# Kernel tuning notes

Hardware: AMD Instinct MI355X
Metric: run time of the kernel (lower is better)

## Reference

```python
import jax, jax.numpy as jnp
import numpy as np

PRE = 4096      # NMS_PRE_MAXSIZE
POST = 512      # NMS_POST_MAXSIZE
THRESH = 0.7    # NMS_THRESH


def setup_inputs() -> dict:
    key = jax.random.key(0)
    k1, k2, k3, k4, k5 = jax.random.split(key, 5)
    B, N, C = 4, 32768, 3
    # realistic lidar-frame boxes: (x, y, z, dx, dy, dz, heading)
    xy = jax.random.uniform(k1, (B, N, 2)) * 140.0 - 70.0
    z = jax.random.uniform(k2, (B, N, 1)) * 3.0 - 2.0
    dims = jax.random.uniform(k3, (B, N, 3)) * 4.0 + 1.0
    heading = jax.random.uniform(k4, (B, N, 1)) * (2.0 * np.pi) - np.pi
    batch_box_preds = jnp.concatenate([xy, z, dims, heading], axis=-1)
    batch_cls_preds = jax.random.normal(k5, (B, N, C))
    return {"batch_cls_preds": batch_cls_preds, "batch_box_preds": batch_box_preds}


def _bev_iou(boxes):
    # boxes: (K, 7); axis-aligned BEV IoU over (x, y, dx, dy) -> (K, K)
    x, y, dx, dy = boxes[:, 0], boxes[:, 1], boxes[:, 3], boxes[:, 4]
    x1, x2 = x - dx * 0.5, x + dx * 0.5
    y1, y2 = y - dy * 0.5, y + dy * 0.5
    ix = jnp.clip(jnp.minimum(x2[:, None], x2[None, :]) - jnp.maximum(x1[:, None], x1[None, :]), 0.0)
    iy = jnp.clip(jnp.minimum(y2[:, None], y2[None, :]) - jnp.maximum(y1[:, None], y1[None, :]), 0.0)
    inter = ix * iy
    area = dx * dy
    union = area[:, None] + area[None, :] - inter
    return inter / jnp.maximum(union, 1e-6)


def _class_agnostic_nms(scores, boxes):
    # scores: (N,), boxes: (N, 7) -> selected idx (POST,), scores (POST,), valid (POST,)
    topk_scores, idx = jax.lax.top_k(scores, PRE)          # score-sorted candidates
    iou = _bev_iou(boxes[idx])                              # (PRE, PRE)
    ar = jnp.arange(PRE)
    def body(i, keep):  # greedy suppression in score order
        sup = keep[i] & (iou[i] > THRESH) & (ar > i)
        return keep & ~sup
    keep = jax.lax.fori_loop(0, PRE, body, jnp.ones((PRE,), bool))
    order = jnp.argsort(jnp.where(keep, ar, PRE))           # stable: kept first, score order
    sel = order[:POST]
    valid = keep[sel]
    return idx[sel], topk_scores[sel] * valid, valid


def reference(batch_cls_preds, batch_box_preds):
    # argmax scoring over classes (torch.max(cls_preds, dim=1))
    roi_scores_all = jnp.max(batch_cls_preds, axis=-1)      # (B, N)
    roi_labels_all = jnp.argmax(batch_cls_preds, axis=-1)   # (B, N)

    def per_item(scores, labels, boxes):
        sel, sel_scores, valid = _class_agnostic_nms(scores, boxes)
        rois = boxes[sel] * valid[:, None].astype(boxes.dtype)   # zero-padded buffer
        roi_labels = jnp.where(valid, labels[sel], 0) + 1        # +1 applied to whole buffer
        return rois, sel_scores, roi_labels

    rois, roi_scores, roi_labels = jax.vmap(per_item)(roi_scores_all, roi_labels_all, batch_box_preds)
    return rois, roi_scores, roi_labels
```

## Files before the change

### kernel.cpp

```cpp
#include <hip/hip_runtime.h>
#include <stdint.h>

typedef unsigned long long u64;

#define BB 4
#define NN 32768
#define CC 3
#define PRE 4096
#define RNK 768
#define POST 512
#define TH 0.7f
#define ROWS_A 768
#define RW (ROWS_A / 64)
#define CANDCAP 2048
#define RS_TILE 2048

__device__ __forceinline__ uint32_t f2u(float f) {
    uint32_t b = __float_as_uint(f);
    return (b & 0x80000000u) ? ~b : (b | 0x80000000u);
}
__device__ __forceinline__ float u2f(uint32_t u) {
    uint32_t b = (u & 0x80000000u) ? (u & 0x7FFFFFFFu) : ~u;
    return __uint_as_float(b);
}
__device__ __forceinline__ float score3(const float* p) {
    return fmaxf(fmaxf(p[0], p[1]), p[2]);
}

__global__ void k_zero(uint4* __restrict__ histreg, uint32_t* __restrict__ scal, int n16) {
    int gid = blockIdx.x * blockDim.x + threadIdx.x;
    if (gid < n16) histreg[gid] = make_uint4(0, 0, 0, 0);
    if (gid < 16) scal[gid] = 0;
}

__global__ void k_hist(const float* __restrict__ cls,
                       uint32_t* __restrict__ hist_f, uint32_t* __restrict__ hist_c) {
    __shared__ uint32_t lc[256];
    lc[threadIdx.x] = 0;
    __syncthreads();
    int gid = blockIdx.x * blockDim.x + threadIdx.x;
    int b = gid >> 15;
    uint32_t p16 = f2u(score3(cls + (size_t)gid * CC)) >> 16;
    atomicAdd(&hist_f[((uint32_t)b << 16) + p16], 1u);
    atomicAdd(&lc[p16 >> 8], 1u);
    __syncthreads();
    uint32_t v = lc[threadIdx.x];
    if (v) atomicAdd(&hist_c[((uint32_t)b << 8) + threadIdx.x], v);
}

__global__ void __launch_bounds__(256) k_collect(const float* __restrict__ cls,
                                                 const uint32_t* __restrict__ hist_c,
                                                 const uint32_t* __restrict__ hist_f,
                                                 uint32_t* __restrict__ cnt,
                                                 uint32_t* __restrict__ ccnt,
                                                 u64* __restrict__ selk, u64* __restrict__ cand) {
    int tid = threadIdx.x;
    int gid = blockIdx.x * 256 + tid;
    int b = gid >> 15;
    __shared__ uint32_t pref[256];
    __shared__ uint32_t s_selc, s_remc, s_pb;

    uint32_t v = hist_c[((uint32_t)b << 8) + 255 - tid];
    pref[tid] = v;
    __syncthreads();
    for (int off = 1; off < 256; off <<= 1) {
        uint32_t x = (tid >= off) ? pref[tid - off] : 0;
        __syncthreads();
        pref[tid] += x;
        __syncthreads();
    }
    {
        uint32_t after = pref[tid], before = after - v;
        if (before < RNK && RNK <= after) { s_selc = 255 - tid; s_remc = RNK - before; }
    }
    __syncthreads();
    uint32_t selc = s_selc, remc = s_remc;
    uint32_t v2 = hist_f[((uint32_t)b << 16) + (selc << 8) + 255 - tid];
    __syncthreads();
    pref[tid] = v2;
    __syncthreads();
    for (int off = 1; off < 256; off <<= 1) {
        uint32_t x = (tid >= off) ? pref[tid - off] : 0;
        __syncthreads();
        pref[tid] += x;
        __syncthreads();
    }
    {
        uint32_t after = pref[tid], before = after - v2;
        if (before < remc && remc <= after) s_pb = (selc << 8) | (uint32_t)(255 - tid);
    }
    __syncthreads();
    uint32_t pb = s_pb;

    u64 k = ((u64)f2u(score3(cls + (size_t)gid * CC)) << 32)
          | (uint32_t)(~(uint32_t)(gid & (NN - 1)));
    uint32_t p16 = (uint32_t)(k >> 48);
    bool def = p16 > pb;
    u64 mask = __ballot(def);
    int lane = tid & 63;
    int wave = tid >> 6;
    __shared__ uint32_t wtot[4], wbase[4], blockbase;
    uint32_t rank = lane ? (uint32_t)__popcll(mask & ((~0ull) >> (64 - lane))) : 0u;
    if (lane == 0) wtot[wave] = (uint32_t)__popcll(mask);
    __syncthreads();
    if (tid == 0) {
        uint32_t t = 0;
        for (int w = 0; w < 4; ++w) { wbase[w] = t; t += wtot[w]; }
        blockbase = atomicAdd(&cnt[b], t);
    }
    __syncthreads();
    if (def) {
        selk[(size_t)b * RNK + blockbase + wbase[wave] + rank] = k;
    } else if (p16 == pb) {
        uint32_t pos = atomicAdd(&ccnt[b], 1u);
        if (pos < CANDCAP) cand[(size_t)b * CANDCAP + pos] = k;
    }
}

__global__ void __launch_bounds__(256) k_rankscatter(const u64* __restrict__ selk,
                                                     const u64* __restrict__ cand,
                                                     const uint32_t* __restrict__ cnt,
                                                     const uint32_t* __restrict__ ccnt,
                                                     const float* __restrict__ box,
                                                     int* __restrict__ sidx,
                                                     float* __restrict__ ssc,
                                                     float* __restrict__ bf) {
    const int bpi = RS_TILE / 64;
    int b = blockIdx.x / bpi;
    int c = blockIdx.x % bpi;
    uint32_t base = cnt[b];
    uint32_t cc = ccnt[b]; if (cc > CANDCAP) cc = CANDCAP;
    uint32_t m = base + cc; if (m > RS_TILE) m = RS_TILE;
    if ((uint32_t)(c * 64) >= m) return;
    __shared__ u64 tile[RS_TILE];
    uint32_t mp = (m + 7) & ~7u;
    for (uint32_t i = threadIdx.x; i < mp; i += 256)
        tile[i] = (i < base) ? selk[(size_t)b * RNK + i]
                : (i < m)    ? cand[(size_t)b * CANDCAP + (i - base)] : 0ull;
    __syncthreads();
    uint32_t k = c * 64 + (threadIdx.x >> 2);
    u64 myk = tile[(k < m) ? k : 0];
    int q = threadIdx.x & 3;
    const ulonglong2* t2 = (const ulonglong2*)tile;
    int cn = 0;
#pragma unroll 8
    for (uint32_t j = 0; j < mp / 8; ++j) {
        ulonglong2 w = t2[4 * j + q];
        cn += (w.x > myk) ? 1 : 0;
        cn += (w.y > myk) ? 1 : 0;
    }
    cn += __shfl_xor(cn, 1, 64);
    cn += __shfl_xor(cn, 2, 64);
    if (q == 0 && k < m && cn < RNK) {
        int r = cn;
        int n = (int)(~(uint32_t)(myk & 0xFFFFFFFFull));
        sidx[b * RNK + r] = n;
        ssc[b * RNK + r] = u2f((uint32_t)(myk >> 32));
        const float* bp = box + ((size_t)b * NN + n) * 7;
        float x = bp[0], y = bp[1], dx = bp[3], dy = bp[4];
        float* bfb = bf + (size_t)b * 5 * RNK;
        bfb[0 * RNK + r] = x - dx * 0.5f;
        bfb[1 * RNK + r] = x + dx * 0.5f;
        bfb[2 * RNK + r] = y - dy * 0.5f;
        bfb[3 * RNK + r] = y + dy * 0.5f;
        bfb[4 * RNK + r] = dx * dy;
    }
}

__global__ void k_iou(const float* __restrict__ bf, u64* __restrict__ supt) {
    const int bpi = ROWS_A / 4;
    int b = blockIdx.x / bpi;
    int wave = threadIdx.x >> 6;
    int lane = threadIdx.x & 63;
    int i = (blockIdx.x % bpi) * 4 + wave;
    const float* bfb = bf + (size_t)b * 5 * RNK;
    float x1 = bfb[0 * RNK + i], x2 = bfb[1 * RNK + i];
    float y1 = bfb[2 * RNK + i], y2 = bfb[3 * RNK + i];
    float ar = bfb[4 * RNK + i];
    u64 myword = 0;
    for (int jw = 0; jw < RW; ++jw) {
        int j = jw * 64 + lane;
        float ix = fminf(x2, bfb[1 * RNK + j]) - fmaxf(x1, bfb[0 * RNK + j]);
        ix = fmaxf(ix, 0.0f);
        float iy = fminf(y2, bfb[3 * RNK + j]) - fmaxf(y1, bfb[2 * RNK + j]);
        iy = fmaxf(iy, 0.0f);
        float inter = __fmul_rn(ix, iy);
        float uni = (ar + bfb[4 * RNK + j]) - inter;
        float iou = inter / fmaxf(uni, 1e-6f);
        u64 bal = __ballot((iou > TH) && (j > i));
        if (jw == lane) myword = bal;
    }
    if (lane < RW) supt[((size_t)b * RW + lane) * ROWS_A + i] = myword;
}

__global__ void __launch_bounds__(1024) k_nmsout(const u64* __restrict__ supt,
                                                 const uint32_t* __restrict__ cnt,
                                                 const uint32_t* __restrict__ ccnt,
                                                 const int* __restrict__ sidx,
                                                 const float* __restrict__ ssc,
                                                 const float* __restrict__ box,
                                                 const float* __restrict__ cls,
                                                 u64* __restrict__ fkey,
                                                 u64* __restrict__ fselk,
                                                 u64* __restrict__ fkr,
                                                 float* __restrict__ fbf,
                                                 float* __restrict__ out) {
    int b = blockIdx.x;
    int tid = threadIdx.x;
    __shared__ u64 keepw[RW], nremw[RW];
    __shared__ uint32_t wpre[65];
    __shared__ int s_changed, s_done;
    const u64* sb = supt + (size_t)b * RW * ROWS_A;

    if (tid < RW) keepw[tid] = ~0ull;
    if (tid == 0) s_done = 0;
    __syncthreads();
    for (int it = 0; it < 48; ++it) {
        if (tid < RW) nremw[tid] = 0;
        if (tid == 0) s_changed = 0;
        __syncthreads();
        for (int tau = tid; tau < ROWS_A; tau += 1024) {
            int w = tau >> 6;
            int r0 = (tau & 63) * 12;
            const u64* wp = sb + (size_t)w * ROWS_A;
            u64 acc = 0;
#pragma unroll
            for (int rr = 0; rr < 12; ++rr) {
                int r = r0 + rr;
                if ((keepw[r >> 6] >> (r & 63)) & 1ull) acc |= wp[r];
            }
            if (acc) atomicOr(&nremw[w], acc);
        }
        __syncthreads();
        if (tid < RW) {
            u64 nk = ~nremw[tid];
            if (nk != keepw[tid]) { s_changed = 1; keepw[tid] = nk; }
        }
        __syncthreads();
        if (!s_changed) { if (tid == 0) s_done = 1; break; }
    }
    __syncthreads();

    if (tid == 0) {
        uint32_t c = 0;
        for (int w = 0; w < RW; ++w) { wpre[w] = c; c += (uint32_t)__popcll(keepw[w]); }
        wpre[RW] = c;
        bool tileok = (cnt[b] + ccnt[b]) <= RS_TILE;
        s_changed = (s_done && c >= POST && tileok) ? 1 : 0;
    }
    __syncthreads();

    if (s_changed) {
        for (int r = tid; r < ROWS_A; r += 1024) {
            int w = r >> 6, bit = r & 63;
            u64 word = keepw[w];
            if (!((word >> bit) & 1ull)) continue;
            u64 mask = bit ? ((1ull << bit) - 1ull) : 0ull;
            uint32_t d = wpre[w] + (uint32_t)__popcll(word & mask);
            if (d < POST) {
                float* ro = out + ((size_t)b * POST + d) * 7;
                int n = sidx[b * RNK + r];
                const float* bp = box + ((size_t)b * NN + n) * 7;
#pragma unroll
                for (int t = 0; t < 7; ++t) ro[t] = bp[t];
                out[(size_t)BB * POST * 7 + b * POST + d] = ssc[b * RNK + r];
                const float* cp = cls + ((size_t)b * NN + n) * CC;
                float c0 = cp[0], c1 = cp[1], c2 = cp[2];
                int lbl = 0; float bst = c0;
                if (c1 > bst) { bst = c1; lbl = 1; }
                if (c2 > bst) { lbl = 2; }
                out[(size_t)BB * POST * 8 + b * POST + d] = (float)(lbl + 1);
            }
        }
        return;
    }

    size_t bo = (size_t)b * NN;
    for (int n = tid; n < NN; n += 1024)
        fkey[bo + n] = ((u64)f2u(score3(cls + (bo + n) * CC)) << 32)
                     | (uint32_t)(~(uint32_t)n);
    __syncthreads();

    __shared__ uint32_t hist[256];
    __shared__ u64 s_prefix;
    __shared__ uint32_t s_k;
    if (tid == 0) { s_prefix = 0; s_k = PRE; }
    __syncthreads();
    for (int pass = 0; pass < 8; ++pass) {
        if (tid < 256) hist[tid] = 0;
        __syncthreads();
        u64 prefix = s_prefix;
        int hi = 8 * pass;
        for (int i = tid; i < NN; i += 1024) {
            u64 k = fkey[bo + i];
            bool match = (pass == 0) || ((k >> (64 - hi)) == prefix);
            if (match) atomicAdd(&hist[(uint32_t)((k >> (56 - hi)) & 255u)], 1u);
        }
        __syncthreads();
        if (tid == 0) {
            uint32_t kneed = s_k, cum = 0; int chosen = 0;
            for (int d = 255; d >= 0; --d) {
                if (kneed <= cum + hist[d]) { chosen = d; break; }
                cum += hist[d];
            }
            s_k = kneed - cum;
            s_prefix = (prefix << 8) | (u64)(uint32_t)chosen;
        }
        __syncthreads();
    }
    u64 kstar = s_prefix;

    __shared__ uint32_t s_cnt;
    if (tid == 0) s_cnt = 0;
    __syncthreads();
    for (int i = tid; i < NN; i += 1024) {
        u64 k = fkey[bo + i];
        if (k >= kstar) {
            uint32_t pos = atomicAdd(&s_cnt, 1u);
            if (pos < PRE) fselk[(size_t)b * PRE + pos] = k;
        }
    }
    __syncthreads();

    __shared__ u64 tile[1024];
    u64 myk0 = fselk[(size_t)b * PRE + tid];
    u64 myk1 = fselk[(size_t)b * PRE + tid + 1024];
    u64 myk2 = fselk[(size_t)b * PRE + tid + 2048];
    u64 myk3 = fselk[(size_t)b * PRE + tid + 3072];
    int rc0 = 0, rc1 = 0, rc2 = 0, rc3 = 0;
    for (int t0 = 0; t0 < PRE; t0 += 1024) {
        tile[tid] = fselk[(size_t)b * PRE + t0 + tid];
        __syncthreads();
#pragma unroll 8
        for (int j = 0; j < 1024; ++j) {
            u64 t = tile[j];
            rc0 += (t > myk0) ? 1 : 0;
            rc1 += (t > myk1) ? 1 : 0;
            rc2 += (t > myk2) ? 1 : 0;
            rc3 += (t > myk3) ? 1 : 0;
        }
        __syncthreads();
    }
    {
        u64 ks[4] = {myk0, myk1, myk2, myk3};
        int rs[4] = {rc0, rc1, rc2, rc3};
#pragma unroll
        for (int j = 0; j < 4; ++j) {
            u64 k = ks[j]; int r = rs[j];
            fkr[(size_t)b * PRE + r] = k;
            int n = (int)(~(uint32_t)(k & 0xFFFFFFFFull));
            const float* bp = box + ((size_t)b * NN + n) * 7;
            float x = bp[0], y = bp[1], dx = bp[3], dy = bp[4];
            float* fb = fbf + (size_t)b * 5 * PRE;
            fb[0 * PRE + r] = x - dx * 0.5f;
            fb[1 * PRE + r] = x + dx * 0.5f;
            fb[2 * PRE + r] = y - dy * 0.5f;
            fb[3 * PRE + r] = y + dy * 0.5f;
            fb[4 * PRE + r] = dx * dy;
        }
    }
    __syncthreads();

    __shared__ u64 km[64];
    const float* fb = fbf + (size_t)b * 5 * PRE;
    if (tid < 64) km[tid] = ~0ull;
    __syncthreads();
    for (int i = 0; i < PRE - 1; ++i) {
        if ((km[i >> 6] >> (i & 63)) & 1ull) {
            float x1 = fb[0 * PRE + i], x2 = fb[1 * PRE + i];
            float y1 = fb[2 * PRE + i], y2 = fb[3 * PRE + i];
            float ar = fb[4 * PRE + i];
            for (int j = i + 1 + tid; j < PRE; j += 1024) {
                float ix = fminf(x2, fb[1 * PRE + j]) - fmaxf(x1, fb[0 * PRE + j]);
                ix = fmaxf(ix, 0.0f);
                float iy = fminf(y2, fb[3 * PRE + j]) - fmaxf(y1, fb[2 * PRE + j]);
                iy = fmaxf(iy, 0.0f);
                float inter = __fmul_rn(ix, iy);
                float uni = (ar + fb[4 * PRE + j]) - inter;
                float iou = inter / fmaxf(uni, 1e-6f);
                if (iou > TH) atomicAnd(&km[j >> 6], ~(1ull << (j & 63)));
            }
        }
        __syncthreads();
    }

    if (tid == 0) {
        uint32_t c = 0;
        for (int w = 0; w < 64; ++w) { wpre[w] = c; c += (uint32_t)__popcll(km[w]); }
        wpre[64] = c;
    }
    __syncthreads();
    uint32_t nkeep = wpre[64];
    for (int r = tid; r < PRE; r += 1024) {
        int w = r >> 6, bit = r & 63;
        u64 word = km[w];
        bool kept = (word >> bit) & 1ull;
        u64 mask = bit ? ((1ull << bit) - 1ull) : 0ull;
        uint32_t before = wpre[w] + (uint32_t)__popcll(word & mask);
        uint32_t d = kept ? before : (nkeep + (uint32_t)r - before);
        if (d < POST) {
            float* ro = out + ((size_t)b * POST + d) * 7;
            float* so = out + (size_t)BB * POST * 7 + b * POST + d;
            float* lo = out + (size_t)BB * POST * 8 + b * POST + d;
            if (kept) {
                u64 k = fkr[(size_t)b * PRE + r];
                int n = (int)(~(uint32_t)(k & 0xFFFFFFFFull));
                const float* bp = box + ((size_t)b * NN + n) * 7;
#pragma unroll
                for (int t = 0; t < 7; ++t) ro[t] = bp[t];
                *so = u2f((uint32_t)(k >> 32));
                const float* cp = cls + ((size_t)b * NN + n) * CC;
                float c0 = cp[0], c1 = cp[1], c2 = cp[2];
                int lbl = 0; float bst = c0;
                if (c1 > bst) { bst = c1; lbl = 1; }
                if (c2 > bst) { lbl = 2; }
                *lo = (float)(lbl + 1);
            } else {
#pragma unroll
                for (int t = 0; t < 7; ++t) ro[t] = 0.0f;
                *so = 0.0f;
                *lo = 1.0f;
            }
        }
    }
}

extern "C" void kernel_launch(void* const* d_in, const int* in_sizes, int n_in,
                              void* d_out, int out_size, void* d_ws, size_t ws_size,
                              hipStream_t stream) {
    const float* cls = (const float*)d_in[0];
    const float* box = (const float*)d_in[1];
    float* out = (float*)d_out;

    char* ws = (char*)d_ws;
    const size_t KB = 1024, MB = 1024 * 1024;
    size_t OFF_SUPT  = 0;
    size_t OFF_HISTF = 512 * KB;
    size_t OFF_HISTC = 1536 * KB;
    size_t OFF_CAND  = 1540 * KB;
    size_t OFF_SELK  = 1604 * KB;
    size_t OFF_BF    = 1664 * KB;
    size_t OFF_SIDX  = 1728 * KB;
    size_t OFF_SSC   = 1740 * KB;
    size_t OFF_SCAL  = 1752 * KB;
    size_t OFF_FKEY  = 2 * MB;
    size_t OFF_FSELK = 3 * MB;
    size_t OFF_FKR   = 3 * MB + 128 * KB;
    size_t OFF_FBF   = 3 * MB + 256 * KB;

    u64*      supt   = (u64*)(ws + OFF_SUPT);
    uint32_t* hist_f = (uint32_t*)(ws + OFF_HISTF);
    uint32_t* hist_c = (uint32_t*)(ws + OFF_HISTC);
    u64*      cand   = (u64*)(ws + OFF_CAND);
    u64*      selk   = (u64*)(ws + OFF_SELK);
    float*    bf     = (float*)(ws + OFF_BF);
    int*      sidx   = (int*)(ws + OFF_SIDX);
    float*    ssc    = (float*)(ws + OFF_SSC);
    uint32_t* scal   = (uint32_t*)(ws + OFF_SCAL);
    uint32_t* cnt    = scal;
    uint32_t* ccnt   = scal + 4;
    u64*      fkey   = (u64*)(ws + OFF_FKEY);
    u64*      fselk  = (u64*)(ws + OFF_FSELK);
    u64*      fkr    = (u64*)(ws + OFF_FKR);
    float*    fbf    = (float*)(ws + OFF_FBF);

    int n16 = (int)((MB + 4 * KB) / 16);
    k_zero<<<(n16 + 255) / 256, 256, 0, stream>>>((uint4*)(ws + OFF_HISTF), scal, n16);
    k_hist<<<(BB * NN) / 256, 256, 0, stream>>>(cls, hist_f, hist_c);
    k_collect<<<(BB * NN) / 256, 256, 0, stream>>>(cls, hist_c, hist_f, cnt, ccnt, selk, cand);
    k_rankscatter<<<BB * (RS_TILE / 64), 256, 0, stream>>>(selk, cand, cnt, ccnt,
                                                           box, sidx, ssc, bf);
    k_iou<<<(ROWS_A / 4) * BB, 256, 0, stream>>>(bf, supt);
    k_nmsout<<<BB, 1024, 0, stream>>>(supt, cnt, ccnt, sidx, ssc, box, cls,
                                      fkey, fselk, fkr, fbf, out);
}
```

Baseline: 64.93 us.

## Replace full-histogram threshold selection with sampled threshold estimate

Drops the zeroing, full 64K-bin histogram and two prefix-scan passes. Instead, one block per batch builds a histogram from the first 2048 scores and picks a threshold expected to pass somewhere between 768 and 2560 elements of the full set. The collect kernel then keeps every score above that threshold using a wave-aggregated atomic, and the rank kernel sorts up to 2560 keys. If the estimate falls outside that range, the existing fallback path in the output kernel is used, which costs more if the sample is unrepresentative.

```diff
diff --git a/kernel.cpp b/kernel.cpp
--- a/kernel.cpp
+++ b/kernel.cpp
@@ -12,8 +12,8 @@
 #define TH 0.7f
 #define ROWS_A 768
 #define RW (ROWS_A / 64)
-#define CANDCAP 2048
-#define RS_TILE 2048
+#define RS_TILE 2560
+#define KPRIME 88
 
 __device__ __forceinline__ uint32_t f2u(float f) {
     uint32_t b = __float_as_uint(f);
@@ -27,100 +27,72 @@
     return fmaxf(fmaxf(p[0], p[1]), p[2]);
 }
 
-__global__ void k_zero(uint4* __restrict__ histreg, uint32_t* __restrict__ scal, int n16) {
-    int gid = blockIdx.x * blockDim.x + threadIdx.x;
-    if (gid < n16) histreg[gid] = make_uint4(0, 0, 0, 0);
-    if (gid < 16) scal[gid] = 0;
-}
-
-__global__ void k_hist(const float* __restrict__ cls,
-                       uint32_t* __restrict__ hist_f, uint32_t* __restrict__ hist_c) {
-    __shared__ uint32_t lc[256];
-    lc[threadIdx.x] = 0;
-    __syncthreads();
+__global__ void __launch_bounds__(256) k_sample(const float* __restrict__ cls,
+                                                uint32_t* __restrict__ scal) {
+    int b = blockIdx.x;
+    int tid = threadIdx.x;
+    __shared__ uint16_t sp[2048];
+    __shared__ uint32_t hist[256];
+    __shared__ uint32_t s_hi, s_rem;
+    for (int s = 0; s < 8; ++s) {
+        int i = s * 256 + tid;
+        sp[i] = (uint16_t)(f2u(score3(cls + ((size_t)b * NN + i) * CC)) >> 16);
+    }
+    hist[tid] = 0;
+    __syncthreads();
+    for (int s = 0; s < 8; ++s) atomicAdd(&hist[sp[s * 256 + tid] >> 8], 1u);
+    __syncthreads();
+    if (tid == 0) {
+        uint32_t need = KPRIME, cum = 0, hb = 0;
+        for (int d = 255; d >= 0; --d) {
+            if (need <= cum + hist[d]) { hb = (uint32_t)d; s_rem = need - cum; break; }
+            cum += hist[d];
+        }
+        s_hi = hb;
+    }
+    __syncthreads();
+    uint32_t hb = s_hi, rem = s_rem;
+    hist[tid] = 0;
+    __syncthreads();
+    for (int s = 0; s < 8; ++s) {
+        uint16_t v = sp[s * 256 + tid];
+        if ((uint32_t)(v >> 8) == hb) atomicAdd(&hist[v & 255], 1u);
+    }
+    __syncthreads();
+    if (tid == 0) {
+        uint32_t need = rem, cum = 0, lb = 0;
+        for (int d = 255; d >= 0; --d) {
+            if (need <= cum + hist[d]) { lb = (uint32_t)d; break; }
+            cum += hist[d];
+        }
+        scal[12 + b] = (hb << 8) | lb;
+        scal[b] = 0;
+    }
+}
+
+__global__ void k_collect(const float* __restrict__ cls, const uint32_t* __restrict__ scal,
+                          uint32_t* __restrict__ cnt, u64* __restrict__ selk) {
     int gid = blockIdx.x * blockDim.x + threadIdx.x;
     int b = gid >> 15;
-    uint32_t p16 = f2u(score3(cls + (size_t)gid * CC)) >> 16;
-    atomicAdd(&hist_f[((uint32_t)b << 16) + p16], 1u);
-    atomicAdd(&lc[p16 >> 8], 1u);
-    __syncthreads();
-    uint32_t v = lc[threadIdx.x];
-    if (v) atomicAdd(&hist_c[((uint32_t)b << 8) + threadIdx.x], v);
-}
-
-__global__ void __launch_bounds__(256) k_collect(const float* __restrict__ cls,
-                                                 const uint32_t* __restrict__ hist_c,
-                                                 const uint32_t* __restrict__ hist_f,
-                                                 uint32_t* __restrict__ cnt,
-                                                 uint32_t* __restrict__ ccnt,
-                                                 u64* __restrict__ selk, u64* __restrict__ cand) {
-    int tid = threadIdx.x;
-    int gid = blockIdx.x * 256 + tid;
-    int b = gid >> 15;
-    __shared__ uint32_t pref[256];
-    __shared__ uint32_t s_selc, s_remc, s_pb;
-
-    uint32_t v = hist_c[((uint32_t)b << 8) + 255 - tid];
-    pref[tid] = v;
-    __syncthreads();
-    for (int off = 1; off < 256; off <<= 1) {
-        uint32_t x = (tid >= off) ? pref[tid - off] : 0;
-        __syncthreads();
-        pref[tid] += x;
-        __syncthreads();
-    }
-    {
-        uint32_t after = pref[tid], before = after - v;
-        if (before < RNK && RNK <= after) { s_selc = 255 - tid; s_remc = RNK - before; }
-    }
-    __syncthreads();
-    uint32_t selc = s_selc, remc = s_remc;
-    uint32_t v2 = hist_f[((uint32_t)b << 16) + (selc << 8) + 255 - tid];
-    __syncthreads();
-    pref[tid] = v2;
-    __syncthreads();
-    for (int off = 1; off < 256; off <<= 1) {
-        uint32_t x = (tid >= off) ? pref[tid - off] : 0;
-        __syncthreads();
-        pref[tid] += x;
-        __syncthreads();
-    }
-    {
-        uint32_t after = pref[tid], before = after - v2;
-        if (before < remc && remc <= after) s_pb = (selc << 8) | (uint32_t)(255 - tid);
-    }
-    __syncthreads();
-    uint32_t pb = s_pb;
-
+    uint32_t pb = scal[12 + b];
     u64 k = ((u64)f2u(score3(cls + (size_t)gid * CC)) << 32)
           | (uint32_t)(~(uint32_t)(gid & (NN - 1)));
-    uint32_t p16 = (uint32_t)(k >> 48);
-    bool def = p16 > pb;
-    u64 mask = __ballot(def);
-    int lane = tid & 63;
-    int wave = tid >> 6;
-    __shared__ uint32_t wtot[4], wbase[4], blockbase;
-    uint32_t rank = lane ? (uint32_t)__popcll(mask & ((~0ull) >> (64 - lane))) : 0u;
-    if (lane == 0) wtot[wave] = (uint32_t)__popcll(mask);
-    __syncthreads();
-    if (tid == 0) {
-        uint32_t t = 0;
-        for (int w = 0; w < 4; ++w) { wbase[w] = t; t += wtot[w]; }
-        blockbase = atomicAdd(&cnt[b], t);
-    }
-    __syncthreads();
-    if (def) {
-        selk[(size_t)b * RNK + blockbase + wbase[wave] + rank] = k;
-    } else if (p16 == pb) {
-        uint32_t pos = atomicAdd(&ccnt[b], 1u);
-        if (pos < CANDCAP) cand[(size_t)b * CANDCAP + pos] = k;
+    bool sel = (uint32_t)(k >> 48) >= pb;
+    u64 mask = __ballot(sel);
+    if (sel) {
+        int lane = threadIdx.x & 63;
+        uint32_t rank = (uint32_t)__popcll(mask & ((1ull << lane) - 1ull));
+        int leader = (int)(__ffsll((long long)mask) - 1);
+        uint32_t base = 0;
+        if (lane == leader) base = atomicAdd(&cnt[b], (uint32_t)__popcll(mask));
+        base = (uint32_t)__shfl((int)base, leader, 64);
+        uint32_t pos = base + rank;
+        if (pos < RS_TILE) selk[(size_t)b * RS_TILE + pos] = k;
     }
 }
 
 __global__ void __launch_bounds__(256) k_rankscatter(const u64* __restrict__ selk,
-                                                     const u64* __restrict__ cand,
                                                      const uint32_t* __restrict__ cnt,
-                                                     const uint32_t* __restrict__ ccnt,
                                                      const float* __restrict__ box,
                                                      int* __restrict__ sidx,
                                                      float* __restrict__ ssc,
@@ -128,15 +100,12 @@
     const int bpi = RS_TILE / 64;
     int b = blockIdx.x / bpi;
     int c = blockIdx.x % bpi;
-    uint32_t base = cnt[b];
-    uint32_t cc = ccnt[b]; if (cc > CANDCAP) cc = CANDCAP;
-    uint32_t m = base + cc; if (m > RS_TILE) m = RS_TILE;
+    uint32_t m = cnt[b]; if (m > RS_TILE) m = RS_TILE;
     if ((uint32_t)(c * 64) >= m) return;
     __shared__ u64 tile[RS_TILE];
     uint32_t mp = (m + 7) & ~7u;
     for (uint32_t i = threadIdx.x; i < mp; i += 256)
-        tile[i] = (i < base) ? selk[(size_t)b * RNK + i]
-                : (i < m)    ? cand[(size_t)b * CANDCAP + (i - base)] : 0ull;
+        tile[i] = (i < m) ? selk[(size_t)b * RS_TILE + i] : 0ull;
     __syncthreads();
     uint32_t k = c * 64 + (threadIdx.x >> 2);
     u64 myk = tile[(k < m) ? k : 0];
@@ -195,7 +164,6 @@
 
 __global__ void __launch_bounds__(1024) k_nmsout(const u64* __restrict__ supt,
                                                  const uint32_t* __restrict__ cnt,
-                                                 const uint32_t* __restrict__ ccnt,
                                                  const int* __restrict__ sidx,
                                                  const float* __restrict__ ssc,
                                                  const float* __restrict__ box,
@@ -245,7 +213,8 @@
         uint32_t c = 0;
         for (int w = 0; w < RW; ++w) { wpre[w] = c; c += (uint32_t)__popcll(keepw[w]); }
         wpre[RW] = c;
-        bool tileok = (cnt[b] + ccnt[b]) <= RS_TILE;
+        uint32_t m = cnt[b];
+        bool tileok = (m >= RNK) && (m <= RS_TILE);
         s_changed = (s_done && c >= POST && tileok) ? 1 : 0;
     }
     __syncthreads();
@@ -435,42 +404,32 @@
     char* ws = (char*)d_ws;
     const size_t KB = 1024, MB = 1024 * 1024;
     size_t OFF_SUPT  = 0;
-    size_t OFF_HISTF = 512 * KB;
-    size_t OFF_HISTC = 1536 * KB;
-    size_t OFF_CAND  = 1540 * KB;
-    size_t OFF_SELK  = 1604 * KB;
-    size_t OFF_BF    = 1664 * KB;
-    size_t OFF_SIDX  = 1728 * KB;
-    size_t OFF_SSC   = 1740 * KB;
-    size_t OFF_SCAL  = 1752 * KB;
+    size_t OFF_SELK  = 512 * KB;
+    size_t OFF_BF    = 640 * KB;
+    size_t OFF_SIDX  = 704 * KB;
+    size_t OFF_SSC   = 716 * KB;
+    size_t OFF_SCAL  = 728 * KB;
     size_t OFF_FKEY  = 2 * MB;
     size_t OFF_FSELK = 3 * MB;
     size_t OFF_FKR   = 3 * MB + 128 * KB;
     size_t OFF_FBF   = 3 * MB + 256 * KB;
 
     u64*      supt   = (u64*)(ws + OFF_SUPT);
-    uint32_t* hist_f = (uint32_t*)(ws + OFF_HISTF);
-    uint32_t* hist_c = (uint32_t*)(ws + OFF_HISTC);
-    u64*      cand   = (u64*)(ws + OFF_CAND);
     u64*      selk   = (u64*)(ws + OFF_SELK);
     float*    bf     = (float*)(ws + OFF_BF);
     int*      sidx   = (int*)(ws + OFF_SIDX);
     float*    ssc    = (float*)(ws + OFF_SSC);
     uint32_t* scal   = (uint32_t*)(ws + OFF_SCAL);
     uint32_t* cnt    = scal;
-    uint32_t* ccnt   = scal + 4;
     u64*      fkey   = (u64*)(ws + OFF_FKEY);
     u64*      fselk  = (u64*)(ws + OFF_FSELK);
     u64*      fkr    = (u64*)(ws + OFF_FKR);
     float*    fbf    = (float*)(ws + OFF_FBF);
 
-    int n16 = (int)((MB + 4 * KB) / 16);
-    k_zero<<<(n16 + 255) / 256, 256, 0, stream>>>((uint4*)(ws + OFF_HISTF), scal, n16);
-    k_hist<<<(BB * NN) / 256, 256, 0, stream>>>(cls, hist_f, hist_c);
-    k_collect<<<(BB * NN) / 256, 256, 0, stream>>>(cls, hist_c, hist_f, cnt, ccnt, selk, cand);
-    k_rankscatter<<<BB * (RS_TILE / 64), 256, 0, stream>>>(selk, cand, cnt, ccnt,
-                                                           box, sidx, ssc, bf);
+    k_sample<<<BB, 256, 0, stream>>>(cls, scal);
+    k_collect<<<(BB * NN) / 256, 256, 0, stream>>>(cls, scal, cnt, selk);
+    k_rankscatter<<<BB * (RS_TILE / 64), 256, 0, stream>>>(selk, cnt, box, sidx, ssc, bf);
     k_iou<<<(ROWS_A / 4) * BB, 256, 0, stream>>>(bf, supt);
-    k_nmsout<<<BB, 1024, 0, stream>>>(supt, cnt, ccnt, sidx, ssc, box, cls,
+    k_nmsout<<<BB, 1024, 0, stream>>>(supt, cnt, sidx, ssc, box, cls,
                                       fkey, fselk, fkr, fbf, out);
 }
```

Measured after the change: 69.77 us. 7.4% more time.
